# Performance work log

Measured on AMD Instinct MI355X. Metric: run time of the kernel, lower is better.

Reference implementation:

```python
import jax, jax.numpy as jnp
import numpy as np

B, N, DIM = 8, 2048, 512
HEADS, DIM_HEAD = 8, 64
INNER = HEADS * DIM_HEAD  # 512
SCALE = DIM_HEAD ** -0.5
NEG = -1e9


def setup_inputs() -> dict:
    key = jax.random.key(0)
    ks = jax.random.split(key, 7)
    x = jax.random.normal(ks[0], (B, N, DIM), dtype=jnp.float32)
    adj = jax.random.uniform(ks[1], (B, N, N), dtype=jnp.float32)
    att_mask = jax.random.randint(ks[2], (B, 1, N, N), 0, 2).astype(jnp.bool_)
    W_gcn = jax.random.normal(ks[3], (DIM, DIM), dtype=jnp.float32) * (DIM ** -0.5)
    W_qkv = jax.random.normal(ks[4], (DIM, 3 * INNER), dtype=jnp.float32) * (DIM ** -0.5)
    W_out = jax.random.normal(ks[5], (INNER + DIM, DIM), dtype=jnp.float32) * ((INNER + DIM) ** -0.5)
    b_out = jax.random.normal(ks[6], (DIM,), dtype=jnp.float32) * 0.01
    return {"x": x, "adj": adj, "att_mask": att_mask,
            "W_gcn": W_gcn, "W_qkv": W_qkv, "W_out": W_out, "b_out": b_out}


def reference(x, adj, att_mask, W_gcn, W_qkv, W_out, b_out):
    # GCN branch: adj @ (x W_gcn)  -> [b, n, dim]
    gcn = jnp.einsum('bnj,bjd->bnd', adj, x @ W_gcn)

    # Attention branch
    qkv = x @ W_qkv                                  # [b, n, 3*inner]
    q, k, v = jnp.split(qkv, 3, axis=-1)
    split_heads = lambda t: t.reshape(B, N, HEADS, DIM_HEAD).transpose(0, 2, 1, 3)
    q, k, v = split_heads(q), split_heads(k), split_heads(v)  # [b, h, n, d]

    dots = jnp.einsum('bhid,bhjd->bhij', q, k) * SCALE        # [b, h, n, n]
    dots = jnp.where(att_mask, NEG, dots)
    attn = jax.nn.softmax(dots, axis=-1)
    att_out = jnp.einsum('bhij,bhjd->bhid', attn, v)          # [b, h, n, d]
    att_out = att_out.transpose(0, 2, 1, 3).reshape(B, N, INNER)

    out = jnp.concatenate([att_out, gcn], axis=-1)            # [b, n, inner+dim]
    return out @ W_out + b_out                                # [b, n, dim]
```

## Files before the change

kernel.cpp:

```cpp
#include <hip/hip_runtime.h>
#include <stdint.h>

#define DEVFN __device__ __forceinline__

typedef __attribute__((ext_vector_type(8))) short short8;
typedef __attribute__((ext_vector_type(4))) short short4v;
typedef __attribute__((ext_vector_type(4))) float floatx4;
typedef __attribute__((ext_vector_type(16))) float floatx16;
typedef __attribute__((ext_vector_type(4))) float vfloat4;
typedef __attribute__((ext_vector_type(2))) unsigned int uint2v;
typedef __attribute__((ext_vector_type(4))) unsigned int uint4v;

#define MFMA_BF16(a,b,c) __builtin_amdgcn_mfma_f32_16x16x32_bf16((a),(b),(c),0,0,0)
#define MFMA32_BF16(a,b,c) __builtin_amdgcn_mfma_f32_32x32x16_bf16((a),(b),(c),0,0,0)
#define GL2LDS(g,l) __builtin_amdgcn_global_load_lds((const __attribute__((address_space(1))) void*)(g), (__attribute__((address_space(3))) void*)(l), 16, 0, 0)

DEVFN unsigned short f2bf(float f){
  unsigned u = __float_as_uint(f);
  u = (u + 0x7fffu + ((u >> 16) & 1u)) >> 16;
  return (unsigned short)u;
}

DEVFN unsigned cvtpk_bf16(float lo, float hi){
  unsigned r;
  asm("v_cvt_pk_bf16_f32 %0, %1, %2" : "=v"(r) : "v"(lo), "v"(hi));
  return r;
}

__global__ void detect_kernel(const unsigned char* m, unsigned int* flag){
  if (threadIdx.x == 0) *flag = 0u;
  __syncthreads();
  int any = 0;
  for (int i = threadIdx.x; i < 4096; i += 256)
    if ((i & 3) != 0 && m[i]) any = 1;
  if (any) atomicOr(flag, 1u);
}

__global__ void prep_small_kernel(const float* __restrict__ x, const float* __restrict__ wg,
                                  const float* __restrict__ wq, const float* __restrict__ wo,
                                  unsigned short* __restrict__ xbf, unsigned short* __restrict__ wcat,
                                  unsigned short* __restrict__ woutT)
{
  int bid = blockIdx.x, tid = threadIdx.x;
  if (bid < 8192) {
    int i = (bid*256 + tid)*4;
    vfloat4 v = *(const vfloat4*)&x[i];
    short4v c; c[0]=(short)f2bf(v[0]); c[1]=(short)f2bf(v[1]); c[2]=(short)f2bf(v[2]); c[3]=(short)f2bf(v[3]);
    *(short4v*)&xbf[i] = c;
  } else if (bid < 12288) {
    int i = (bid - 8192)*256 + tid;
    int k = i & 511, c = i >> 9;
    float v = (c < 512) ? wg[k*512 + c] : wq[k*1536 + (c - 512)];
    if (c >= 512 && c < 1024) v *= 0.18033688f;
    wcat[c*512 + k] = (unsigned short)f2bf(v);
  } else {
    int i = (bid - 12288)*256 + tid;
    int k = i & 1023, n2 = i >> 10;
    woutT[n2*1024 + k] = (unsigned short)f2bf(wo[k*512 + n2]);
  }
}

__global__ void prep_full_kernel(const float* __restrict__ x, const float* __restrict__ wg,
                                 const float* __restrict__ wq, const float* __restrict__ wo,
                                 const void* __restrict__ mask, const unsigned* __restrict__ flag,
                                 unsigned short* __restrict__ xbf, unsigned short* __restrict__ wcat,
                                 unsigned short* __restrict__ woutT, unsigned* __restrict__ mp)
{
  int bid = blockIdx.x, tid = threadIdx.x;
  if (bid < 8192) {
    int i = (bid*256 + tid)*4;
    vfloat4 v = *(const vfloat4*)&x[i];
    short4v c; c[0]=(short)f2bf(v[0]); c[1]=(short)f2bf(v[1]); c[2]=(short)f2bf(v[2]); c[3]=(short)f2bf(v[3]);
    *(short4v*)&xbf[i] = c;
  } else if (bid < 12288) {
    int i = (bid - 8192)*256 + tid;
    int k = i & 511, c = i >> 9;
    float v = (c < 512) ? wg[k*512 + c] : wq[k*1536 + (c - 512)];
    if (c >= 512 && c < 1024) v *= 0.18033688f;
    wcat[c*512 + k] = (unsigned short)f2bf(v);
  } else if (bid < 14336) {
    int i = (bid - 12288)*256 + tid;
    int k = i & 1023, n2 = i >> 10;
    woutT[n2*1024 + k] = (unsigned short)f2bf(wo[k*512 + n2]);
  } else {
    int j = bid - 14336;
    int e = j*256 + tid;
    int v;
    if (*flag) v = ((const unsigned char*)mask)[e];
    else       v = ((const int*)mask)[e];
    unsigned long long ball = __ballot(v != 0);
    int base = e & ~63;
    int lane = tid & 63;
    if (lane == 0)  mp[(base >> 5) + 0] = (unsigned)(ball & 0xffffffffull);
    if (lane == 32) mp[(base >> 5) + 1] = (unsigned)(ball >> 32);
  }
}

DEVFN void gemm_kloop_bf16(const unsigned short* Ag, int lda,
                           const unsigned short* Bg, int ldb, int K,
                           short* As, short* Bs, int w, int l,
                           floatx4 (&acc)[4][4])
{
  const int wr = (w >> 1)*64, wc = (w & 1)*64;
  for (int k0 = 0; k0 < K; k0 += 32) {
    __syncthreads();
#pragma unroll
    for (int i = 0; i < 2; i++) {
      int id = (w*2 + i)*64 + l;
      int row = id >> 2, part = id & 3;
      GL2LDS(Ag + row*lda + k0 + part*8, As + (w*2 + i)*512);
      GL2LDS(Bg + row*ldb + k0 + part*8, Bs + (w*2 + i)*512);
    }
    __syncthreads();
    short8 af[4], bfr[4];
#pragma unroll
    for (int t = 0; t < 4; t++) {
      af[t]  = *(const short8*)&As[(wr + t*16 + (l & 15))*32 + ((l >> 4) << 3)];
      bfr[t] = *(const short8*)&Bs[(wc + t*16 + (l & 15))*32 + ((l >> 4) << 3)];
    }
#pragma unroll
    for (int a2 = 0; a2 < 4; a2++)
#pragma unroll
      for (int b2 = 0; b2 < 4; b2++)
        acc[a2][b2] = MFMA_BF16(af[a2], bfr[b2], acc[a2][b2]);
  }
}

__global__ __launch_bounds__(256, 2)
void gemm_ab_kernel(const unsigned short* __restrict__ xbf, const unsigned short* __restrict__ wcat,
                    unsigned short* __restrict__ xgT, unsigned short* __restrict__ Qo,
                    unsigned short* __restrict__ Ko, unsigned short* __restrict__ VTo,
                    const void* __restrict__ mask, const unsigned* __restrict__ flag,
                    const float* __restrict__ adj,
                    unsigned* __restrict__ mp, unsigned short* __restrict__ adjb,
                    int mode)
{
  __shared__ short lds[16384];
  int tid = threadIdx.x, w = tid >> 6, l = tid & 63;
  int bid = blockIdx.x;

  int gemmid;
  if (mode) {
    int r11 = bid % 11, g11 = bid / 11;
    if (r11 != 0) {
      int bw = g11*10 + (r11 - 1);
      if (bw < 16384) {
        unsigned fl = *flag;
        int lane = tid & 63;
        int vv[8];
        if (fl) {
          const unsigned char* m8 = (const unsigned char*)mask;
#pragma unroll
          for (int j = 0; j < 8; j++) vv[j] = m8[(bw*8 + j)*256 + tid];
        } else {
          const int* m32 = (const int*)mask;
#pragma unroll
          for (int j = 0; j < 8; j++) vv[j] = m32[(bw*8 + j)*256 + tid];
        }
#pragma unroll
        for (int j = 0; j < 8; j++) {
          unsigned long long ball = __ballot(vv[j] != 0);
          int e = (bw*8 + j)*256 + tid;
          int base = e & ~63;
          if (lane == 0)  mp[(base >> 5) + 0] = (unsigned)(ball & 0xffffffffull);
          if (lane == 32) mp[(base >> 5) + 1] = (unsigned)(ball >> 32);
        }
      } else {
        int ab = bw - 16384;
        vfloat4 vv[8];
#pragma unroll
        for (int j = 0; j < 8; j++)
          vv[j] = *(const vfloat4*)&adj[((ab*8 + j)*256 + tid)*4];
#pragma unroll
        for (int j = 0; j < 8; j++) {
          short4v c; c[0]=(short)f2bf(vv[j][0]); c[1]=(short)f2bf(vv[j][1]);
          c[2]=(short)f2bf(vv[j][2]); c[3]=(short)f2bf(vv[j][3]);
          *(short4v*)&adjb[((ab*8 + j)*256 + tid)*4] = c;
        }
      }
      return;
    }
    gemmid = g11;
  } else {
    gemmid = bid;
  }

  int xcd = gemmid & 7, slot = gemmid >> 3;
  int p  = xcd + ((slot >> 4) << 3);
  int nt = slot & 15;
  int rows0 = p*128, cols0 = nt*128;

  floatx4 acc[4][4];
  const floatx4 zf = {0.f, 0.f, 0.f, 0.f};
#pragma unroll
  for (int a2 = 0; a2 < 4; a2++)
#pragma unroll
    for (int b2 = 0; b2 < 4; b2++) acc[a2][b2] = zf;

  gemm_kloop_bf16(xbf + rows0*512, 512, wcat + cols0*512, 512, 512,
                  lds, lds + 4096, w, l, acc);
  __syncthreads();

  int wr = (w >> 1)*64, wc = (w & 1)*64;
  int b = p >> 4;
  int n0 = (p & 15)*128 + wr;
  int gc0 = cols0 + wc;

  if (nt < 4 || nt >= 12) {
    short* T = lds + w*4096;
#pragma unroll
    for (int mi = 0; mi < 4; mi++)
#pragma unroll
      for (int bi = 0; bi < 4; bi++)
#pragma unroll
        for (int r = 0; r < 4; r++) {
          int rl = mi*16 + ((l >> 4) << 2) + r;
          int cl = bi*16 + (l & 15);
          T[cl*64 + ((((rl >> 3) ^ (cl & 7))) << 3) + (rl & 7)] = (short)f2bf(acc[mi][bi][r]);
        }
#pragma unroll
    for (int i = 0; i < 8; i++) {
      int chunk = i*64 + l;
      int c = chunk >> 3, s = chunk & 7;
      short8 v = *(const short8*)&T[c*64 + ((s ^ (c & 7)) << 3)];
      int rowstart = n0 + s*8;
      if (nt < 4) {
        int d = gc0 + c;
        *(short8*)&xgT[(b*512 + d)*2048 + rowstart] = v;
      } else {
        int vc = gc0 + c - 1536;
        int hh = vc >> 6, dd = vc & 63;
        *(short8*)&VTo[((b*8 + hh)*64 + dd)*2048 + rowstart] = v;
      }
    }
  } else {
    unsigned short* dst = (nt < 8) ? Qo : Ko;
    int cbase = gc0 - ((nt < 8) ? 512 : 1024);
    int hh = cbase >> 6;
#pragma unroll
    for (int mi = 0; mi < 4; mi++)
#pragma unroll
      for (int bi = 0; bi < 4; bi++)
#pragma unroll
        for (int r = 0; r < 4; r++) {
          int rowg = n0 + mi*16 + ((l >> 4) << 2) + r;
          int dd = bi*16 + (l & 15);
          dst[((b*8 + hh)*2048 + rowg)*64 + dd] = (unsigned short)f2bf(acc[mi][bi][r]);
        }
  }
}

__global__ __launch_bounds__(256, 2)
void gemm_c_f32_kernel(const float* __restrict__ adj, const unsigned short* __restrict__ xgT,
                       unsigned short* __restrict__ cat)
{
  __shared__ short lds[8192];
  int tid = threadIdx.x, w = tid >> 6, l = tid & 63;
  int bid = blockIdx.x;
  int xcd = bid & 7, slot = bid >> 3;
  int p  = xcd + ((slot >> 2) << 3);
  int nt = slot & 3;
  int b = p >> 4, mt = p & 15;
  int rows0 = mt*128, cols0 = nt*128;
  const float* Ag = adj + (size_t)b*2048*2048 + (size_t)rows0*2048;
  const unsigned short* Bg = xgT + (b*512 + cols0)*2048;

  floatx4 acc[4][4];
  const floatx4 zf = {0.f, 0.f, 0.f, 0.f};
#pragma unroll
  for (int a2 = 0; a2 < 4; a2++)
#pragma unroll
    for (int b2 = 0; b2 < 4; b2++) acc[a2][b2] = zf;

  const int wr = (w >> 1)*64, wc = (w & 1)*64;
  for (int k0 = 0; k0 < 2048; k0 += 32) {
    __syncthreads();
#pragma unroll
    for (int i = 0; i < 4; i++) {
      int id = (w*4 + i)*64 + l;
      int row = id >> 3, part = id & 7;
      vfloat4 v = *(const vfloat4*)&Ag[row*2048 + k0 + part*4];
      short4v c4; c4[0]=(short)f2bf(v[0]); c4[1]=(short)f2bf(v[1]); c4[2]=(short)f2bf(v[2]); c4[3]=(short)f2bf(v[3]);
      *(short4v*)&lds[row*32 + part*4] = c4;
    }
#pragma unroll
    for (int i = 0; i < 2; i++) {
      int id = (w*2 + i)*64 + l;
      int row = id >> 2, part = id & 3;
      GL2LDS(Bg + row*2048 + k0 + part*8, lds + 4096 + (w*2 + i)*512);
    }
    __syncthreads();
    short8 af[4], bfr[4];
#pragma unroll
    for (int t = 0; t < 4; t++) {
      af[t]  = *(const short8*)&lds[(wr + t*16 + (l & 15))*32 + ((l >> 4) << 3)];
      bfr[t] = *(const short8*)&lds[4096 + (wc + t*16 + (l & 15))*32 + ((l >> 4) << 3)];
    }
#pragma unroll
    for (int a2 = 0; a2 < 4; a2++)
#pragma unroll
      for (int b2 = 0; b2 < 4; b2++)
        acc[a2][b2] = MFMA_BF16(af[a2], bfr[b2], acc[a2][b2]);
  }

#pragma unroll
  for (int mi = 0; mi < 4; mi++)
#pragma unroll
    for (int bi = 0; bi < 4; bi++)
#pragma unroll
      for (int r = 0; r < 4; r++) {
        int rowg = b*2048 + rows0 + wr + mi*16 + ((l >> 4) << 2) + r;
        int col  = 512 + cols0 + wc + bi*16 + (l & 15);
        cat[rowg*1024 + col] = (unsigned short)f2bf(acc[mi][bi][r]);
      }
}

DEVFN void attn_stage(const unsigned short* KB, const unsigned short* VB,
                      short* Ks, short* Vs, int kn0, int w, int l)
{
#pragma unroll
  for (int i = 0; i < 2; i++) {
    int id = (w*2 + i)*64 + l;
    int row = id >> 3, sl = id & 7;
    int sp = sl ^ (row & 7) ^ (((row >> 3) & 3) << 1);
    GL2LDS(KB + (kn0 + row)*64 + sp*8, Ks + (w*2 + i)*512);
    GL2LDS(VB + row*2048 + kn0 + sp*8, Vs + (w*2 + i)*512);
  }
}

DEVFN void attn_body(int abid, short* lds,
                     const unsigned short* __restrict__ Q, const unsigned short* __restrict__ Kb,
                     const unsigned short* __restrict__ VT, const unsigned* __restrict__ mp,
                     unsigned short* __restrict__ cat)
{
  int tid = threadIdx.x, w = tid >> 6, l = tid & 63;
  int c5 = l & 31, h = l >> 5;
  int hv = h*4;

  int xcd = abid & 7, slot = abid >> 3;
  int bh = xcd + ((slot >> 4) << 3);
  int qt = slot & 15;
  int b = bh >> 3, hd = bh & 7;
  int qw = qt*128 + w*32;

  const unsigned short* Qb = Q  + (size_t)bh*2048*64;
  const unsigned short* KB = Kb + (size_t)bh*2048*64;
  const unsigned short* VB = VT + (size_t)bh*64*2048;
  const unsigned* mrow = mp + b*2048*64 + (qw + c5)*64;

  short8 qf[4];
#pragma unroll
  for (int dk = 0; dk < 4; dk++)
    qf[dk] = *(const short8*)&Qb[(qw + c5)*64 + dk*16 + h*8];

  int koff[2][4], voff[2][2][2];
#pragma unroll
  for (int kb = 0; kb < 2; kb++) {
    int row = kb*32 + c5;
    int rsw = (row & 7) ^ (((row >> 3) & 3) << 1);
#pragma unroll
    for (int dk = 0; dk < 4; dk++)
      koff[kb][dk] = (row*64 + (((dk*2 + h) ^ rsw) << 3))*2;
  }
#pragma unroll
  for (int db = 0; db < 2; db++) {
    int vrow = db*32 + c5;
    int vsw = (vrow & 7) ^ (((vrow >> 3) & 3) << 1);
#pragma unroll
    for (int kb = 0; kb < 2; kb++)
#pragma unroll
      for (int ksl = 0; ksl < 2; ksl++)
        voff[kb][ksl][db] = (vrow*64 + (((kb*4 + ksl*2 + h) ^ vsw) << 3))*2;
  }

  floatx16 oacc0, oacc1, nacc;
  const floatx16 zf16 = {0.f,0.f,0.f,0.f,0.f,0.f,0.f,0.f,0.f,0.f,0.f,0.f,0.f,0.f,0.f,0.f};
  oacc0 = zf16; oacc1 = zf16; nacc = zf16;

  const short8 ones8 = {(short)0x3F80,(short)0x3F80,(short)0x3F80,(short)0x3F80,
                        (short)0x3F80,(short)0x3F80,(short)0x3F80,(short)0x3F80};

  auto do_tile = [&](const short* Ks, const short* Vs, uint2v wdt) {
#pragma unroll
    for (int kb = 0; kb < 2; kb++) {
      floatx16 sacc;
      __builtin_amdgcn_s_setprio(1);
      {
        short8 kf = *(const short8*)((const char*)Ks + koff[kb][0]);
        sacc = MFMA32_BF16(kf, qf[0], zf16);
      }
#pragma unroll
      for (int dk = 1; dk < 4; dk++) {
        short8 kf = *(const short8*)((const char*)Ks + koff[kb][dk]);
        sacc = MFMA32_BF16(kf, qf[dk], sacc);
      }
      __builtin_amdgcn_s_setprio(0);

      unsigned keep = ~((kb ? wdt.y : wdt.x) >> hv);
      float ps[16];
#pragma unroll
      for (int t = 0; t < 16; t++) {
        int pos = (t >> 2)*8 + (t & 3);
        int keepm = __builtin_amdgcn_sbfe((int)keep, pos, 1);
        float p = exp2f(sacc[t]);
        ps[t] = __uint_as_float(__float_as_uint(p) & (unsigned)keepm);
      }
      unsigned pk[4][2];
#pragma unroll
      for (int s = 0; s < 4; s++) {
        pk[s][0] = cvtpk_bf16(ps[s*4 + 0], ps[s*4 + 1]);
        pk[s][1] = cvtpk_bf16(ps[s*4 + 2], ps[s*4 + 3]);
      }
#pragma unroll
      for (int ksl = 0; ksl < 2; ksl++) {
        uint2v s0 = __builtin_amdgcn_permlane32_swap(pk[2*ksl][0], pk[2*ksl + 1][0], false, false);
        uint2v s1 = __builtin_amdgcn_permlane32_swap(pk[2*ksl][1], pk[2*ksl + 1][1], false, false);
        uint4v fu;
        fu[0] = s0.x; fu[1] = s1.x; fu[2] = s0.y; fu[3] = s1.y;
        short8 pfrag = *(short8*)&fu;

        __builtin_amdgcn_s_setprio(1);
        {
          short8 vf = *(const short8*)((const char*)Vs + voff[kb][ksl][0]);
          oacc0 = MFMA32_BF16(pfrag, vf, oacc0);
        }
        {
          short8 vf = *(const short8*)((const char*)Vs + voff[kb][ksl][1]);
          oacc1 = MFMA32_BF16(pfrag, vf, oacc1);
        }
        nacc = MFMA32_BF16(pfrag, ones8, nacc);
        __builtin_amdgcn_s_setprio(0);
      }
    }
  };

  attn_stage(KB, VB, lds, lds + 8192, 0, w, l);
  uint2v wd = *(const uint2v*)&mrow[0];
  asm volatile("s_waitcnt vmcnt(0)" ::: "memory");
  __builtin_amdgcn_s_barrier();
  asm volatile("" ::: "memory");

  for (int t2 = 0; t2 < 16; t2++) {
    attn_stage(KB, VB, lds + 4096, lds + 12288, (2*t2 + 1)*64, w, l);
    uint2v wdB = *(const uint2v*)&mrow[(2*t2 + 1)*2];

    do_tile(lds, lds + 8192, wd);

    asm volatile("s_waitcnt vmcnt(0)" ::: "memory");
    __builtin_amdgcn_s_barrier();
    asm volatile("" ::: "memory");

    uint2v wdN = wd;
    if (t2 < 15) {
      attn_stage(KB, VB, lds, lds + 8192, (2*t2 + 2)*64, w, l);
      wdN = *(const uint2v*)&mrow[(2*t2 + 2)*2];
    }

    do_tile(lds + 4096, lds + 12288, wdB);
    wd = wdN;

    asm volatile("s_waitcnt vmcnt(0)" ::: "memory");
    __builtin_amdgcn_s_barrier();
    asm volatile("" ::: "memory");
  }

#pragma unroll
  for (int t = 0; t < 16; t++) {
    float iv = 1.0f / nacc[t];
    int qrow = qw + (t & 3) + 8*(t >> 2) + hv;
    unsigned short* orow = &cat[(b*2048 + qrow)*1024 + hd*64];
    orow[c5]      = (unsigned short)f2bf(oacc0[t] * iv);
    orow[32 + c5] = (unsigned short)f2bf(oacc1[t] * iv);
  }
}

__global__ __launch_bounds__(256, 4)
void attn_kernel(const unsigned short* __restrict__ Q, const unsigned short* __restrict__ Kb,
                 const unsigned short* __restrict__ VT, const unsigned* __restrict__ mp,
                 unsigned short* __restrict__ cat)
{
  __shared__ short lds[16384];
  attn_body(blockIdx.x, lds, Q, Kb, VT, mp, cat);
}

__global__ __launch_bounds__(256, 4)
void fused_ca_kernel(const unsigned short* __restrict__ adjb, const unsigned short* __restrict__ xgT,
                     const unsigned short* __restrict__ Q, const unsigned short* __restrict__ Kb,
                     const unsigned short* __restrict__ VT, const unsigned* __restrict__ mp,
                     unsigned short* __restrict__ cat)
{
  __shared__ short lds[16384];
  int bid = blockIdx.x;
  int r3 = bid % 3;
  if (r3 == 2) {
    int cbid = bid / 3;
    int tid = threadIdx.x, w = tid >> 6, l = tid & 63;
    int xcd = cbid & 7, slot = cbid >> 3;
    int p  = xcd + ((slot >> 2) << 3);
    int nt = slot & 3;
    int b = p >> 4, mt = p & 15;
    int rows0 = mt*128, cols0 = nt*128;

    floatx4 acc[4][4];
    const floatx4 zf = {0.f, 0.f, 0.f, 0.f};
#pragma unroll
    for (int a2 = 0; a2 < 4; a2++)
#pragma unroll
      for (int b2 = 0; b2 < 4; b2++) acc[a2][b2] = zf;

    gemm_kloop_bf16(adjb + (size_t)b*2048*2048 + (size_t)rows0*2048, 2048,
                    xgT + (b*512 + cols0)*2048, 2048, 2048,
                    lds, lds + 4096, w, l, acc);

    int wr = (w >> 1)*64, wc = (w & 1)*64;
#pragma unroll
    for (int mi = 0; mi < 4; mi++)
#pragma unroll
      for (int bi = 0; bi < 4; bi++)
#pragma unroll
        for (int r = 0; r < 4; r++) {
          int rowg = b*2048 + rows0 + wr + mi*16 + ((l >> 4) << 2) + r;
          int col  = 512 + cols0 + wc + bi*16 + (l & 15);
          cat[rowg*1024 + col] = (unsigned short)f2bf(acc[mi][bi][r]);
        }
  } else {
    int abid = (bid / 3)*2 + r3;
    attn_body(abid, lds, Q, Kb, VT, mp, cat);
  }
}

__global__ __launch_bounds__(256, 2)
void gemm_d_kernel(const unsigned short* __restrict__ cat, const unsigned short* __restrict__ woutT,
                   const float* __restrict__ bout, float* __restrict__ out)
{
  __shared__ short lds[8192];
  int tid = threadIdx.x, w = tid >> 6, l = tid & 63;
  int bid = blockIdx.x;
  int xcd = bid & 7, slot = bid >> 3;
  int p  = xcd + ((slot >> 2) << 3);
  int nt = slot & 3;
  int rows0 = p*128, cols0 = nt*128;

  floatx4 acc[4][4];
  const floatx4 zf = {0.f, 0.f, 0.f, 0.f};
#pragma unroll
  for (int a2 = 0; a2 < 4; a2++)
#pragma unroll
    for (int b2 = 0; b2 < 4; b2++) acc[a2][b2] = zf;

  gemm_kloop_bf16(cat + (size_t)rows0*1024, 1024, woutT + cols0*1024, 1024, 1024,
                  lds, lds + 4096, w, l, acc);

  int wr = (w >> 1)*64, wc = (w & 1)*64;
#pragma unroll
  for (int bi = 0; bi < 4; bi++) {
    int col = cols0 + wc + bi*16 + (l & 15);
    float bias = bout[col];
#pragma unroll
    for (int mi = 0; mi < 4; mi++)
#pragma unroll
      for (int r = 0; r < 4; r++) {
        int rowg = rows0 + wr + mi*16 + ((l >> 4) << 2) + r;
        out[rowg*512 + col] = acc[mi][bi][r] + bias;
      }
  }
}

extern "C" void kernel_launch(void* const* d_in, const int* in_sizes, int n_in,
                              void* d_out, int out_size, void* d_ws, size_t ws_size,
                              hipStream_t stream)
{
  (void)in_sizes; (void)n_in; (void)out_size;
  const float* x   = (const float*)d_in[0];
  const float* adj = (const float*)d_in[1];
  const void*  msk = d_in[2];
  const float* wg  = (const float*)d_in[3];
  const float* wq  = (const float*)d_in[4];
  const float* wo  = (const float*)d_in[5];
  const float* bo  = (const float*)d_in[6];
  float* out = (float*)d_out;
  char* ws = (char*)d_ws;

  unsigned short* xbf   = (unsigned short*)(ws + 0);
  unsigned short* wcat  = (unsigned short*)(ws + 16777216);
  unsigned short* woutT = (unsigned short*)(ws + 18874368);
  unsigned short* xgT   = (unsigned short*)(ws + 19922944);
  unsigned short* Qb    = (unsigned short*)(ws + 36700160);
  unsigned short* Kb    = (unsigned short*)(ws + 53477376);
  unsigned short* VTb   = (unsigned short*)(ws + 70254592);
  unsigned short* cat   = (unsigned short*)(ws + 87031808);
  unsigned*       mp    = (unsigned*)(ws + 120586240);
  unsigned*       flag  = (unsigned*)(ws + 124780544);
  unsigned short* adjb  = (unsigned short*)(ws + 124780608);

  const int use_adjb = (ws_size >= (size_t)124780608 + 67108864) ? 1 : 0;

  detect_kernel<<<1, 256, 0, stream>>>((const unsigned char*)msk, flag);
  if (use_adjb) {
    prep_small_kernel<<<14336, 256, 0, stream>>>(x, wg, wq, wo, xbf, wcat, woutT);
    gemm_ab_kernel<<<22528, 256, 0, stream>>>(xbf, wcat, xgT, Qb, Kb, VTb,
                                              msk, flag, adj, mp, adjb, 1);
    fused_ca_kernel<<<1536, 256, 0, stream>>>(adjb, xgT, Qb, Kb, VTb, mp, cat);
  } else {
    prep_full_kernel<<<145408, 256, 0, stream>>>(x, wg, wq, wo, msk, flag,
                                                 xbf, wcat, woutT, mp);
    gemm_ab_kernel<<<2048, 256, 0, stream>>>(xbf, wcat, xgT, Qb, Kb, VTb,
                                             msk, flag, adj, mp, adjb, 0);
    gemm_c_f32_kernel<<<512, 256, 0, stream>>>(adj, xgT, cat);
    attn_kernel<<<1024, 256, 0, stream>>>(Qb, Kb, VTb, mp, cat);
  }
  gemm_d_kernel<<<512, 256, 0, stream>>>(cat, woutT, bo, out);
}
```

Measured before the change: 362.7 us.

## Double-buffer only K in attention, single-buffer V, raise occupancy

The attention loop is split into a QK^T plus softmax phase and a PV phase. Only K stays double-buffered in LDS. V is single-buffered and loaded at the start of each tile, so it overlaps only with that tile's QK^T work. This cuts LDS per block from 32KB to 24KB, and launch bounds are raised from 4 to 6 to allow more resident blocks. The costs are an extra barrier per key tile, a shorter prefetch distance for V, and tighter register limits that may cause spills.

```diff
diff --git a/kernel.cpp b/kernel.cpp
--- a/kernel.cpp
+++ b/kernel.cpp
@@ -315,8 +315,7 @@
       }
 }
 
-DEVFN void attn_stage(const unsigned short* KB, const unsigned short* VB,
-                      short* Ks, short* Vs, int kn0, int w, int l)
+DEVFN void attn_stage_k(const unsigned short* KB, short* Ks, int kn0, int w, int l)
 {
 #pragma unroll
   for (int i = 0; i < 2; i++) {
@@ -324,6 +323,16 @@
     int row = id >> 3, sl = id & 7;
     int sp = sl ^ (row & 7) ^ (((row >> 3) & 3) << 1);
     GL2LDS(KB + (kn0 + row)*64 + sp*8, Ks + (w*2 + i)*512);
+  }
+}
+
+DEVFN void attn_stage_v(const unsigned short* VB, short* Vs, int kn0, int w, int l)
+{
+#pragma unroll
+  for (int i = 0; i < 2; i++) {
+    int id = (w*2 + i)*64 + l;
+    int row = id >> 3, sl = id & 7;
+    int sp = sl ^ (row & 7) ^ (((row >> 3) & 3) << 1);
     GL2LDS(VB + row*2048 + kn0 + sp*8, Vs + (w*2 + i)*512);
   }
 }
@@ -348,6 +357,10 @@
   const unsigned short* VB = VT + (size_t)bh*64*2048;
   const unsigned* mrow = mp + b*2048*64 + (qw + c5)*64;
 
+  short* K0 = lds;
+  short* K1 = lds + 4096;
+  short* Vb = lds + 8192;
+
   short8 qf[4];
 #pragma unroll
   for (int dk = 0; dk < 4; dk++)
@@ -380,7 +393,7 @@
   const short8 ones8 = {(short)0x3F80,(short)0x3F80,(short)0x3F80,(short)0x3F80,
                         (short)0x3F80,(short)0x3F80,(short)0x3F80,(short)0x3F80};
 
-  auto do_tile = [&](const short* Ks, const short* Vs, uint2v wdt) {
+  auto do_qkt_sm = [&](const short* Ks, uint2v wdt, unsigned (&pk)[2][4][2]) {
 #pragma unroll
     for (int kb = 0; kb < 2; kb++) {
       floatx16 sacc;
@@ -405,27 +418,32 @@
         float p = exp2f(sacc[t]);
         ps[t] = __uint_as_float(__float_as_uint(p) & (unsigned)keepm);
       }
-      unsigned pk[4][2];
 #pragma unroll
       for (int s = 0; s < 4; s++) {
-        pk[s][0] = cvtpk_bf16(ps[s*4 + 0], ps[s*4 + 1]);
-        pk[s][1] = cvtpk_bf16(ps[s*4 + 2], ps[s*4 + 3]);
-      }
+        pk[kb][s][0] = cvtpk_bf16(ps[s*4 + 0], ps[s*4 + 1]);
+        pk[kb][s][1] = cvtpk_bf16(ps[s*4 + 2], ps[s*4 + 3]);
+      }
+    }
+  };
+
+  auto do_pv = [&](unsigned (&pk)[2][4][2]) {
+#pragma unroll
+    for (int kb = 0; kb < 2; kb++) {
 #pragma unroll
       for (int ksl = 0; ksl < 2; ksl++) {
-        uint2v s0 = __builtin_amdgcn_permlane32_swap(pk[2*ksl][0], pk[2*ksl + 1][0], false, false);
-        uint2v s1 = __builtin_amdgcn_permlane32_swap(pk[2*ksl][1], pk[2*ksl + 1][1], false, false);
+        uint2v s0 = __builtin_amdgcn_permlane32_swap(pk[kb][2*ksl][0], pk[kb][2*ksl + 1][0], false, false);
+        uint2v s1 = __builtin_amdgcn_permlane32_swap(pk[kb][2*ksl][1], pk[kb][2*ksl + 1][1], false, false);
         uint4v fu;
         fu[0] = s0.x; fu[1] = s1.x; fu[2] = s0.y; fu[3] = s1.y;
         short8 pfrag = *(short8*)&fu;
 
         __builtin_amdgcn_s_setprio(1);
         {
-          short8 vf = *(const short8*)((const char*)Vs + voff[kb][ksl][0]);
+          short8 vf = *(const short8*)((const char*)Vb + voff[kb][ksl][0]);
           oacc0 = MFMA32_BF16(pfrag, vf, oacc0);
         }
         {
-          short8 vf = *(const short8*)((const char*)Vs + voff[kb][ksl][1]);
+          short8 vf = *(const short8*)((const char*)Vb + voff[kb][ksl][1]);
           oacc1 = MFMA32_BF16(pfrag, vf, oacc1);
         }
         nacc = MFMA32_BF16(pfrag, ones8, nacc);
@@ -434,34 +452,37 @@
     }
   };
 
-  attn_stage(KB, VB, lds, lds + 8192, 0, w, l);
+  attn_stage_k(KB, K0, 0, w, l);
   uint2v wd = *(const uint2v*)&mrow[0];
   asm volatile("s_waitcnt vmcnt(0)" ::: "memory");
   __builtin_amdgcn_s_barrier();
   asm volatile("" ::: "memory");
 
-  for (int t2 = 0; t2 < 16; t2++) {
-    attn_stage(KB, VB, lds + 4096, lds + 12288, (2*t2 + 1)*64, w, l);
-    uint2v wdB = *(const uint2v*)&mrow[(2*t2 + 1)*2];
-
-    do_tile(lds, lds + 8192, wd);
+  unsigned pk[2][4][2];
+
+  for (int kt = 0; kt < 32; kt++) {
+    const short* Kcur = (kt & 1) ? K1 : K0;
+    short* Knext      = (kt & 1) ? K0 : K1;
+
+    attn_stage_v(VB, Vb, kt*64, w, l);
+    uint2v wdn = wd;
+    if (kt < 31) {
+      attn_stage_k(KB, Knext, (kt + 1)*64, w, l);
+      wdn = *(const uint2v*)&mrow[(kt + 1)*2];
+    }
+
+    do_qkt_sm(Kcur, wd, pk);
 
     asm volatile("s_waitcnt vmcnt(0)" ::: "memory");
     __builtin_amdgcn_s_barrier();
     asm volatile("" ::: "memory");
 
-    uint2v wdN = wd;
-    if (t2 < 15) {
-      attn_stage(KB, VB, lds, lds + 8192, (2*t2 + 2)*64, w, l);
-      wdN = *(const uint2v*)&mrow[(2*t2 + 2)*2];
-    }
-
-    do_tile(lds + 4096, lds + 12288, wdB);
-    wd = wdN;
-
-    asm volatile("s_waitcnt vmcnt(0)" ::: "memory");
+    do_pv(pk);
+
     __builtin_amdgcn_s_barrier();
     asm volatile("" ::: "memory");
+
+    wd = wdn;
   }
 
 #pragma unroll
@@ -474,22 +495,22 @@
   }
 }
 
-__global__ __launch_bounds__(256, 4)
+__global__ __launch_bounds__(256, 6)
 void attn_kernel(const unsigned short* __restrict__ Q, const unsigned short* __restrict__ Kb,
                  const unsigned short* __restrict__ VT, const unsigned* __restrict__ mp,
                  unsigned short* __restrict__ cat)
 {
-  __shared__ short lds[16384];
+  __shared__ short lds[12288];
   attn_body(blockIdx.x, lds, Q, Kb, VT, mp, cat);
 }
 
-__global__ __launch_bounds__(256, 4)
+__global__ __launch_bounds__(256, 6)
 void fused_ca_kernel(const unsigned short* __restrict__ adjb, const unsigned short* __restrict__ xgT,
                      const unsigned short* __restrict__ Q, const unsigned short* __restrict__ Kb,
                      const unsigned short* __restrict__ VT, const unsigned* __restrict__ mp,
                      unsigned short* __restrict__ cat)
 {
-  __shared__ short lds[16384];
+  __shared__ short lds[12288];
   int bid = blockIdx.x;
   int r3 = bid % 3;
   if (r3 == 2) {
```

Measured after the change: 1.018 ms. 181% more time.
